# Kernel tuning notes

Measured on AMD Instinct MI355X. Metric: run time of the kernel, lower is better.

The kernel has to match this reference:

```python
import jax, jax.numpy as jnp
import numpy as np

T, DIM, HID = 8192, 1024, 4096

def setup_inputs() -> dict:
    key = jax.random.key(0)
    k1, k2, k3 = jax.random.split(key, 3)
    x = jax.random.normal(k1, (T, DIM), dtype=jnp.float32)
    # torch Linear weight layout: [out_features, in_features]
    W_fc = jax.random.normal(k2, (HID, DIM), dtype=jnp.float32) * 0.02
    W_proj = jax.random.normal(k3, (DIM, HID), dtype=jnp.float32) * 0.02
    return {"x": x, "W_fc": W_fc, "W_proj": W_proj}

def reference(x, W_fc, W_proj):
    # fc: x @ W_fc^T  -> relu -> square -> proj: @ W_proj^T
    h = jnp.einsum('td,hd->th', x, W_fc)      # [T, HID]
    h = jnp.square(jax.nn.relu(h))            # relu(h)^2 (relu^2 activation)
    return jnp.einsum('th,dh->td', h, W_proj) # [T, DIM]
```

## Files before the change

### kernel.cpp

```cpp
#include <hip/hip_runtime.h>
#include <stdint.h>


#define BM 128
#define BN 128
#define BK 32

typedef __attribute__((ext_vector_type(8))) short bf16x8;
typedef __attribute__((ext_vector_type(4))) float f32x4;

typedef const __attribute__((address_space(1))) unsigned int* gas_u32p;
typedef __attribute__((address_space(3))) unsigned int* las_u32p;

__device__ __forceinline__ void load16_to_lds(const void* gptr, void* lptr) {
    __builtin_amdgcn_global_load_lds((gas_u32p)gptr, (las_u32p)lptr, 16, 0, 0);
}

__device__ __forceinline__ unsigned short f2bf(float f) {
    unsigned int u = __float_as_uint(f);
    u += 0x7FFFu + ((u >> 16) & 1u);
    return (unsigned short)(u >> 16);
}

__global__ void cvt_f32_bf16(const float4* __restrict__ src,
                             ushort4* __restrict__ dst, int n4)
{
    int i = blockIdx.x * blockDim.x + threadIdx.x;
    int stride = gridDim.x * blockDim.x;
    for (; i < n4; i += stride) {
        float4 v = src[i];
        ushort4 o;
        o.x = f2bf(v.x); o.y = f2bf(v.y); o.z = f2bf(v.z); o.w = f2bf(v.w);
        dst[i] = o;
    }
}

template<bool RELU2, bool OUT_BF16>
__global__ __launch_bounds__(256, 3)
void gemm_bt(const unsigned short* __restrict__ A,
             const unsigned short* __restrict__ B,
             void* __restrict__ Cv, int M, int N, int K)
{
    __shared__ unsigned short sA[BM * BK];
    __shared__ unsigned short sB[BN * BK];

    const int tid  = threadIdx.x;
    const int lane = tid & 63;
    const int wave = tid >> 6;
    const int wm   = (wave >> 1) * 64;
    const int wn   = (wave & 1) * 64;
    const int quad = lane >> 4;
    const int m16  = lane & 15;

    const long bm0 = (long)blockIdx.y * BM;
    const long bn0 = (long)blockIdx.x * BN;

    const int srow = tid >> 2;
    const int scol = (tid & 3) * 8;

    const unsigned short* gA = A + (bm0 + srow) * (long)K + scol;
    const unsigned short* gB = B + (bn0 + srow) * (long)K + scol;
    char* lA = (char*)sA + tid * 16;
    char* lB = (char*)sB + tid * 16;

    f32x4 acc[4][4];
    #pragma unroll
    for (int i = 0; i < 4; i++)
        #pragma unroll
        for (int j = 0; j < 4; j++)
            acc[i][j] = (f32x4)0.0f;

    for (int k0 = 0; k0 < K; k0 += BK) {
        load16_to_lds(gA + k0,                lA);
        load16_to_lds(gA + 64 * (long)K + k0, lA + 4096);
        load16_to_lds(gB + k0,                lB);
        load16_to_lds(gB + 64 * (long)K + k0, lB + 4096);
        __syncthreads();

        bf16x8 af[4], bfr[4];
        #pragma unroll
        for (int i = 0; i < 4; i++)
            af[i]  = *(const bf16x8*)&sA[(wm + i * 16 + m16) * BK + quad * 8];
        #pragma unroll
        for (int j = 0; j < 4; j++)
            bfr[j] = *(const bf16x8*)&sB[(wn + j * 16 + m16) * BK + quad * 8];

        #pragma unroll
        for (int i = 0; i < 4; i++)
            #pragma unroll
            for (int j = 0; j < 4; j++)
                acc[i][j] = __builtin_amdgcn_mfma_f32_16x16x32_bf16(
                    af[i], bfr[j], acc[i][j], 0, 0, 0);

        __syncthreads();
    }

    #pragma unroll
    for (int i = 0; i < 4; i++) {
        #pragma unroll
        for (int j = 0; j < 4; j++) {
            #pragma unroll
            for (int r = 0; r < 4; r++) {
                float v = acc[i][j][r];
                if (RELU2) v = (v > 0.0f) ? v * v : 0.0f;
                const long row = bm0 + wm + i * 16 + quad * 4 + r;
                const long col = bn0 + wn + j * 16 + m16;
                if (OUT_BF16)
                    ((unsigned short*)Cv)[row * (long)N + col] = f2bf(v);
                else
                    ((float*)Cv)[row * (long)N + col] = v;
            }
        }
    }
}

extern "C" void kernel_launch(void* const* d_in, const int* in_sizes, int n_in,
                              void* d_out, int out_size, void* d_ws, size_t ws_size,
                              hipStream_t stream) {
    (void)in_sizes; (void)n_in; (void)out_size; (void)ws_size;

    const int T = 8192, DIM = 1024, HID = 4096;

    const float* x     = (const float*)d_in[0];
    const float* W_fc  = (const float*)d_in[1];
    const float* W_prj = (const float*)d_in[2];
    float* out = (float*)d_out;

    char* ws = (char*)d_ws;
    unsigned short* h   = (unsigned short*)ws;
    unsigned short* xb  = (unsigned short*)(ws + (64l << 20));
    unsigned short* wfb = (unsigned short*)(ws + (80l << 20));
    unsigned short* wpb = (unsigned short*)(ws + (88l << 20));

    const int nx = T * DIM / 4, nw1 = HID * DIM / 4, nw2 = DIM * HID / 4;
    cvt_f32_bf16<<<1024, 256, 0, stream>>>((const float4*)x,     (ushort4*)xb,  nx);
    cvt_f32_bf16<<<1024, 256, 0, stream>>>((const float4*)W_fc,  (ushort4*)wfb, nw1);
    cvt_f32_bf16<<<1024, 256, 0, stream>>>((const float4*)W_prj, (ushort4*)wpb, nw2);

    gemm_bt<true, true><<<dim3(HID / BN, T / BM), dim3(256), 0, stream>>>(
        xb, wfb, h, T, HID, DIM);

    gemm_bt<false, false><<<dim3(DIM / BN, T / BM), dim3(256), 0, stream>>>(
        h, wpb, out, T, DIM, HID);
}
```

Measured before the change: 276.6 us.

## Fuse fp32-to-bf16 conversion into GEMM loads with register-staged double buffering

Removes the three separate conversion kernels and instead loads fp32 inputs straight into registers inside the GEMM, packs them to bf16 and stores them to a double-buffered LDS tile. The next tile is prefetched into registers while MFMAs run on the current buffer, and block indices are remapped per XCD to improve L2 locality. This drops the extra conversion passes and launches. In exchange, fp32 weights are re-read and re-converted by every block that uses them, and register pressure rises.

```diff
diff --git a/kernel.cpp b/kernel.cpp
--- a/kernel.cpp
+++ b/kernel.cpp
@@ -9,40 +9,22 @@
 typedef __attribute__((ext_vector_type(8))) short bf16x8;
 typedef __attribute__((ext_vector_type(4))) float f32x4;
 
-typedef const __attribute__((address_space(1))) unsigned int* gas_u32p;
-typedef __attribute__((address_space(3))) unsigned int* las_u32p;
-
-__device__ __forceinline__ void load16_to_lds(const void* gptr, void* lptr) {
-    __builtin_amdgcn_global_load_lds((gas_u32p)gptr, (las_u32p)lptr, 16, 0, 0);
-}
-
 __device__ __forceinline__ unsigned short f2bf(float f) {
     unsigned int u = __float_as_uint(f);
     u += 0x7FFFu + ((u >> 16) & 1u);
     return (unsigned short)(u >> 16);
 }
-
-__global__ void cvt_f32_bf16(const float4* __restrict__ src,
-                             ushort4* __restrict__ dst, int n4)
-{
-    int i = blockIdx.x * blockDim.x + threadIdx.x;
-    int stride = gridDim.x * blockDim.x;
-    for (; i < n4; i += stride) {
-        float4 v = src[i];
-        ushort4 o;
-        o.x = f2bf(v.x); o.y = f2bf(v.y); o.z = f2bf(v.z); o.w = f2bf(v.w);
-        dst[i] = o;
-    }
+__device__ __forceinline__ unsigned int pack2(float lo, float hi) {
+    return (unsigned int)f2bf(lo) | ((unsigned int)f2bf(hi) << 16);
 }
 
-template<bool RELU2, bool OUT_BF16>
+template<bool AF32, bool BF32, bool RELU2, bool OUTBF16, int SWIZ>
 __global__ __launch_bounds__(256, 3)
-void gemm_bt(const unsigned short* __restrict__ A,
-             const unsigned short* __restrict__ B,
+void gemm_bt(const void* __restrict__ Av, const void* __restrict__ Bv,
              void* __restrict__ Cv, int M, int N, int K)
 {
-    __shared__ unsigned short sA[BM * BK];
-    __shared__ unsigned short sB[BN * BK];
+    __shared__ unsigned short sA[2][BM * BK];
+    __shared__ unsigned short sB[2][BN * BK];
 
     const int tid  = threadIdx.x;
     const int lane = tid & 63;
@@ -52,16 +34,71 @@
     const int quad = lane >> 4;
     const int m16  = lane & 15;
 
-    const long bm0 = (long)blockIdx.y * BM;
-    const long bn0 = (long)blockIdx.x * BN;
+    const int lbid = blockIdx.y * gridDim.x + blockIdx.x;
+    int bx, by;
+    if (SWIZ == 1) {
+        const int xcd = lbid & 7, t = lbid >> 3;
+        bx = (xcd & 3) * 2 + (t & 1);
+        by = (xcd >> 2) * 32 + (t >> 1);
+    } else {
+        const int xcd = lbid & 7, t = lbid >> 3;
+        by = xcd * 8 + (t & 7);
+        bx = t >> 3;
+    }
 
-    const int srow = tid >> 2;
-    const int scol = (tid & 3) * 8;
+    const long bm0 = (long)by * BM;
+    const long bn0 = (long)bx * BN;
 
-    const unsigned short* gA = A + (bm0 + srow) * (long)K + scol;
-    const unsigned short* gB = B + (bn0 + srow) * (long)K + scol;
-    char* lA = (char*)sA + tid * 16;
-    char* lB = (char*)sB + tid * 16;
+    const unsigned short* gAb = (const unsigned short*)Av + (bm0 + (tid >> 2)) * (long)K + (tid & 3) * 8;
+    const float*          gAf = (const float*)Av          + (bm0 + (tid >> 3)) * (long)K + (tid & 7) * 4;
+    const unsigned short* gBb = (const unsigned short*)Bv + (bn0 + (tid >> 2)) * (long)K + (tid & 3) * 8;
+    const float*          gBf = (const float*)Bv          + (bn0 + (tid >> 3)) * (long)K + (tid & 7) * 4;
+
+    uint4  rab[2]; float4 raf[4];
+    uint4  rbb[2]; float4 rbf[4];
+
+    auto loadA = [&](int k0) {
+        if constexpr (AF32) {
+            #pragma unroll
+            for (int j = 0; j < 4; j++) raf[j] = *(const float4*)(gAf + (long)j * 32 * K + k0);
+        } else {
+            #pragma unroll
+            for (int j = 0; j < 2; j++) rab[j] = *(const uint4*)(gAb + (long)j * 64 * K + k0);
+        }
+    };
+    auto loadB = [&](int k0) {
+        if constexpr (BF32) {
+            #pragma unroll
+            for (int j = 0; j < 4; j++) rbf[j] = *(const float4*)(gBf + (long)j * 32 * K + k0);
+        } else {
+            #pragma unroll
+            for (int j = 0; j < 2; j++) rbb[j] = *(const uint4*)(gBb + (long)j * 64 * K + k0);
+        }
+    };
+    auto writeA = [&](int p) {
+        if constexpr (AF32) {
+            #pragma unroll
+            for (int j = 0; j < 4; j++) {
+                uint2 w; w.x = pack2(raf[j].x, raf[j].y); w.y = pack2(raf[j].z, raf[j].w);
+                *(uint2*)&sA[p][((tid >> 3) + j * 32) * BK + (tid & 7) * 4] = w;
+            }
+        } else {
+            *(uint4*)&sA[p][tid * 8]        = rab[0];
+            *(uint4*)&sA[p][tid * 8 + 2048] = rab[1];
+        }
+    };
+    auto writeB = [&](int p) {
+        if constexpr (BF32) {
+            #pragma unroll
+            for (int j = 0; j < 4; j++) {
+                uint2 w; w.x = pack2(rbf[j].x, rbf[j].y); w.y = pack2(rbf[j].z, rbf[j].w);
+                *(uint2*)&sB[p][((tid >> 3) + j * 32) * BK + (tid & 7) * 4] = w;
+            }
+        } else {
+            *(uint4*)&sB[p][tid * 8]        = rbb[0];
+            *(uint4*)&sB[p][tid * 8 + 2048] = rbb[1];
+        }
+    };
 
     f32x4 acc[4][4];
     #pragma unroll
@@ -70,20 +107,23 @@
         for (int j = 0; j < 4; j++)
             acc[i][j] = (f32x4)0.0f;
 
-    for (int k0 = 0; k0 < K; k0 += BK) {
-        load16_to_lds(gA + k0,                lA);
-        load16_to_lds(gA + 64 * (long)K + k0, lA + 4096);
-        load16_to_lds(gB + k0,                lB);
-        load16_to_lds(gB + 64 * (long)K + k0, lB + 4096);
-        __syncthreads();
+    const int nk = K / BK;
+
+    loadA(0); loadB(0);
+    writeA(0); writeB(0);
+    __syncthreads();
+    if (nk > 1) { loadA(BK); loadB(BK); }
+
+    for (int k0 = 0; k0 < nk; k0++) {
+        const int p = k0 & 1;
 
         bf16x8 af[4], bfr[4];
         #pragma unroll
         for (int i = 0; i < 4; i++)
-            af[i]  = *(const bf16x8*)&sA[(wm + i * 16 + m16) * BK + quad * 8];
+            af[i]  = *(const bf16x8*)&sA[p][(wm + i * 16 + m16) * BK + quad * 8];
         #pragma unroll
         for (int j = 0; j < 4; j++)
-            bfr[j] = *(const bf16x8*)&sB[(wn + j * 16 + m16) * BK + quad * 8];
+            bfr[j] = *(const bf16x8*)&sB[p][(wn + j * 16 + m16) * BK + quad * 8];
 
         #pragma unroll
         for (int i = 0; i < 4; i++)
@@ -92,7 +132,13 @@
                 acc[i][j] = __builtin_amdgcn_mfma_f32_16x16x32_bf16(
                     af[i], bfr[j], acc[i][j], 0, 0, 0);
 
+        if (k0 + 1 < nk) {
+            writeA(p ^ 1); writeB(p ^ 1);
+        }
         __syncthreads();
+        if (k0 + 2 < nk) {
+            loadA((k0 + 2) * BK); loadB((k0 + 2) * BK);
+        }
     }
 
     #pragma unroll
@@ -105,7 +151,7 @@
                 if (RELU2) v = (v > 0.0f) ? v * v : 0.0f;
                 const long row = bm0 + wm + i * 16 + quad * 4 + r;
                 const long col = bn0 + wn + j * 16 + m16;
-                if (OUT_BF16)
+                if (OUTBF16)
                     ((unsigned short*)Cv)[row * (long)N + col] = f2bf(v);
                 else
                     ((float*)Cv)[row * (long)N + col] = v;
@@ -126,20 +172,11 @@
     const float* W_prj = (const float*)d_in[2];
     float* out = (float*)d_out;
 
-    char* ws = (char*)d_ws;
-    unsigned short* h   = (unsigned short*)ws;
-    unsigned short* xb  = (unsigned short*)(ws + (64l << 20));
-    unsigned short* wfb = (unsigned short*)(ws + (80l << 20));
-    unsigned short* wpb = (unsigned short*)(ws + (88l << 20));
+    unsigned short* h = (unsigned short*)d_ws;
 
-    const int nx = T * DIM / 4, nw1 = HID * DIM / 4, nw2 = DIM * HID / 4;
-    cvt_f32_bf16<<<1024, 256, 0, stream>>>((const float4*)x,     (ushort4*)xb,  nx);
-    cvt_f32_bf16<<<1024, 256, 0, stream>>>((const float4*)W_fc,  (ushort4*)wfb, nw1);
-    cvt_f32_bf16<<<1024, 256, 0, stream>>>((const float4*)W_prj, (ushort4*)wpb, nw2);
+    gemm_bt<true, true, true, true, 0>
+        <<<dim3(HID / BN, T / BM), dim3(256), 0, stream>>>(x, W_fc, h, T, HID, DIM);
 
-    gemm_bt<true, true><<<dim3(HID / BN, T / BM), dim3(256), 0, stream>>>(
-        xb, wfb, h, T, HID, DIM);
-
-    gemm_bt<false, false><<<dim3(DIM / BN, T / BM), dim3(256), 0, stream>>>(
-        h, wpb, out, T, DIM, HID);
+    gemm_bt<false, true, false, false, 1>
+        <<<dim3(DIM / BN, T / BM), dim3(256), 0, stream>>>(h, W_prj, out, T, DIM, HID);
 }
```

After: 413.7 us. 49.6% more time.
